# Kernel tuning notes

Hardware: AMD Instinct MI355X
Metric: run time of the kernel (lower is better)

## Reference

```python
import jax, jax.numpy as jnp
import numpy as np

IN_FEATURES = 28 * 28  # 784
OUT_FEATURES = 1000    # label_num
GRID_SIZE = 10
SPLINE_ORDER = 3
GRID_RANGE = (0.0, 1.0)


def _make_grid(dtype):
    # grid = arange(-spline_order, grid_size+spline_order+1) * h + grid_range[0]
    h = (GRID_RANGE[1] - GRID_RANGE[0]) / GRID_SIZE
    return (jnp.arange(-SPLINE_ORDER, GRID_SIZE + SPLINE_ORDER + 1, dtype=dtype) * h
            + GRID_RANGE[0])  # [grid_size + 2*spline_order + 1] = [17]


def b_splines(x):
    # x: [B, in]; returns [B, in, grid_size + spline_order] = [B, 784, 13]
    grid = _make_grid(x.dtype)
    g = grid[None, None, :]          # broadcast over batch and in_features
    xu = x[:, :, None]               # [B, in, 1]
    bases = ((xu >= g[..., :-1]) & (xu < g[..., 1:])).astype(x.dtype)
    for k in range(1, SPLINE_ORDER + 1):
        left = (xu - g[..., :-(k + 1)]) / (g[..., k:-1] - g[..., :-(k + 1)])
        right = (g[..., k + 1:] - xu) / (g[..., k + 1:] - g[..., 1:-k])
        bases = left * bases[..., :-1] + right * bases[..., 1:]
    return bases


def setup_inputs() -> dict:
    key = jax.random.key(0)
    k1, k2, k3, k4 = jax.random.split(key, 4)
    B = 8192
    x = jax.random.uniform(k1, (B, 1, 28, 28), dtype=jnp.float32)  # values in grid range [0,1]
    base_weight = 0.03 * jax.random.normal(k2, (OUT_FEATURES, IN_FEATURES), dtype=jnp.float32)
    spline_weight = 0.02 * jax.random.normal(
        k3, (OUT_FEATURES, IN_FEATURES, GRID_SIZE + SPLINE_ORDER), dtype=jnp.float32)
    spline_scaler = 1.0 + 0.05 * jax.random.normal(k4, (OUT_FEATURES, IN_FEATURES), dtype=jnp.float32)
    return {"x": x, "base_weight": base_weight,
            "spline_weight": spline_weight, "spline_scaler": spline_scaler}


def reference(x, base_weight, spline_weight, spline_scaler):
    B = x.shape[0]
    xf = x.reshape(B, IN_FEATURES)                       # Flatten
    # base branch: SiLU(x) @ base_weight.T
    base_out = jnp.einsum('bi,oi->bo', jax.nn.silu(xf), base_weight)
    # spline branch: B-spline basis contracted with scaled spline weights
    bases = b_splines(xf)                                # [B, in, 13]
    sw = spline_weight * spline_scaler[..., None]        # [out, in, 13]
    spline_out = jnp.einsum('big,oig->bo', bases, sw)
    logits = base_out + spline_out                       # [B, out]
    return jax.nn.log_softmax(logits, axis=1)
```

## Files before the change

kernel.cpp:

```cpp
#include <hip/hip_runtime.h>
#include <hip/hip_bf16.h>
#include <stdint.h>

#define IN_F 784
#define OUT_F 1000
#define CH 16
#define KDIM (IN_F * CH)
#define MDIM 8192
#define NPAD 1024
#define NT (KDIM / 64)
#define BUFSZ 49152

typedef __attribute__((ext_vector_type(8))) short bf16x8;
typedef __attribute__((ext_vector_type(4))) float f32x4;

__device__ __forceinline__ unsigned short f2bf(float f) {
    unsigned u = __float_as_uint(f);
    u = (u + 0x7FFFu + ((u >> 16) & 1u)) >> 16;
    return (unsigned short)u;
}
__device__ __forceinline__ unsigned pack2(float lo, float hi) {
    return (unsigned)f2bf(lo) | ((unsigned)f2bf(hi) << 16);
}

__global__ void prep_A(const float* __restrict__ X, unsigned short* __restrict__ A) {
    int tid = blockIdx.x * 256 + threadIdx.x;
    int b = tid / IN_F;
    int i = tid - b * IN_F;
    float x = X[tid];
    float s = x / (1.0f + __expf(-x));
    float tf = x * 10.0f;
    float cf = floorf(tf);
    cf = fminf(fmaxf(cf, 0.0f), 9.0f);
    int c = (int)cf;
    float u = tf - cf;
    float u2 = u * u, u3 = u2 * u;
    float om = 1.0f - u;
    const float s6 = 1.0f / 6.0f;
    float b0 = om * om * om * s6;
    float b1 = (3.0f * u3 - 6.0f * u2 + 4.0f) * s6;
    float b2 = (-3.0f * u3 + 3.0f * u2 + 3.0f * u + 1.0f) * s6;
    float b3 = u3 * s6;
    float v[16];
    v[0] = s;
    #pragma unroll
    for (int k = 0; k < 13; ++k) {
        float val = (k == c)     ? b0 : 0.0f;
        val       = (k == c + 1) ? b1 : val;
        val       = (k == c + 2) ? b2 : val;
        val       = (k == c + 3) ? b3 : val;
        v[1 + k] = val;
    }
    v[14] = 0.0f; v[15] = 0.0f;
    unsigned w[8];
    #pragma unroll
    for (int j = 0; j < 8; ++j) w[j] = pack2(v[2 * j], v[2 * j + 1]);
    uint4* dst = (uint4*)(A + (size_t)b * KDIM + (size_t)i * CH);
    dst[0] = make_uint4(w[0], w[1], w[2], w[3]);
    dst[1] = make_uint4(w[4], w[5], w[6], w[7]);
}

__global__ void prep_W(const float* __restrict__ BW, const float* __restrict__ SW,
                       const float* __restrict__ SC, unsigned short* __restrict__ Wm) {
    int tid = blockIdx.x * 256 + threadIdx.x;
    int o = tid / IN_F;
    int i = tid - o * IN_F;
    unsigned w[8];
    if (o < OUT_F) {
        float bw = BW[o * IN_F + i];
        float sc = SC[o * IN_F + i];
        const float* swp = SW + (size_t)(o * IN_F + i) * 13;
        float v[16];
        v[0] = bw;
        #pragma unroll
        for (int g = 0; g < 13; ++g) v[1 + g] = swp[g] * sc;
        v[14] = 0.0f; v[15] = 0.0f;
        #pragma unroll
        for (int j = 0; j < 8; ++j) w[j] = pack2(v[2 * j], v[2 * j + 1]);
    } else {
        #pragma unroll
        for (int j = 0; j < 8; ++j) w[j] = 0u;
    }
    uint4* dst = (uint4*)(Wm + (size_t)o * KDIM + (size_t)i * CH);
    dst[0] = make_uint4(w[0], w[1], w[2], w[3]);
    dst[1] = make_uint4(w[4], w[5], w[6], w[7]);
}

__global__ void __launch_bounds__(512, 2) kan_gemm(const unsigned short* __restrict__ A,
                                                   const unsigned short* __restrict__ W,
                                                   float* __restrict__ out) {
    __shared__ __align__(16) unsigned char smem[3 * BUFSZ];
    const int t = threadIdx.x;
    const int bid = blockIdx.x;
    const int sid = ((bid & 7) << 5) + (bid >> 3);
    const int mb = sid >> 3, nb = sid & 7;
    const int bRow = mb << 8, bCol = nb << 7;

    const int lane = t & 63;
    const int w    = t >> 6;
    const int lrow = lane & 15;
    const int lk   = lane >> 4;
    const int sx   = lrow & 7;
    const int wm   = w >> 1, wn = w & 1;
    const int r8   = t >> 3;
    const int p    = t & 7;
    const int lch  = p ^ (r8 & 7);

    const char* srcA[4];
    const char* srcB[2];
    #pragma unroll
    for (int it = 0; it < 4; ++it)
        srcA[it] = (const char*)A + ((size_t)(bRow + it * 64 + r8) * KDIM) * 2 + lch * 16;
    #pragma unroll
    for (int it = 0; it < 2; ++it)
        srcB[it] = (const char*)W + ((size_t)(bCol + it * 64 + r8) * KDIM) * 2 + lch * 16;

    auto stage = [&](int kt, int buf) {
        const size_t ko = (size_t)kt << 7;
        const unsigned db = buf * BUFSZ + t * 16;
        #pragma unroll
        for (int it = 0; it < 4; ++it)
            __builtin_amdgcn_global_load_lds(
                (const __attribute__((address_space(1))) char*)(srcA[it] + ko),
                (__attribute__((address_space(3))) char*)&smem[db + it * 8192],
                16, 0, 0);
        #pragma unroll
        for (int it = 0; it < 2; ++it)
            __builtin_amdgcn_global_load_lds(
                (const __attribute__((address_space(1))) char*)(srcB[it] + ko),
                (__attribute__((address_space(3))) char*)&smem[db + 32768 + it * 8192],
                16, 0, 0);
    };

    f32x4 acc[4][4];
    #pragma unroll
    for (int m = 0; m < 4; ++m)
        #pragma unroll
        for (int n = 0; n < 4; ++n)
            acc[m][n] = (f32x4){0.f, 0.f, 0.f, 0.f};

    stage(0, 0);
    stage(1, 1);

    int cur = 0;
    int nbf = 2;
    for (int kt = 0; kt < NT; ++kt) {
        if (kt < NT - 1) asm volatile("s_waitcnt vmcnt(6)" ::: "memory");
        else             asm volatile("s_waitcnt vmcnt(0)" ::: "memory");
        __builtin_amdgcn_s_barrier();
        asm volatile("" ::: "memory");

        const unsigned char* Abuf = &smem[cur * BUFSZ];
        const unsigned char* Bbuf = Abuf + 32768;
        bf16x8 af[4][2], bfr[4][2];
        #pragma unroll
        for (int m = 0; m < 4; ++m) {
            const int row = (wm << 6) + (m << 4) + lrow;
            #pragma unroll
            for (int kk = 0; kk < 2; ++kk)
                af[m][kk] = *(const bf16x8*)&Abuf[row * 128 + (((kk << 2) + lk) ^ sx) * 16];
        }
        #pragma unroll
        for (int n = 0; n < 4; ++n) {
            const int row = (wn << 6) + (n << 4) + lrow;
            #pragma unroll
            for (int kk = 0; kk < 2; ++kk)
                bfr[n][kk] = *(const bf16x8*)&Bbuf[row * 128 + (((kk << 2) + lk) ^ sx) * 16];
        }

        if (kt + 2 < NT) stage(kt + 2, nbf);

        __builtin_amdgcn_s_setprio(1);
        #pragma unroll
        for (int m = 0; m < 4; ++m)
            #pragma unroll
            for (int n = 0; n < 4; ++n) {
                acc[m][n] = __builtin_amdgcn_mfma_f32_16x16x32_bf16(af[m][0], bfr[n][0], acc[m][n], 0, 0, 0);
                acc[m][n] = __builtin_amdgcn_mfma_f32_16x16x32_bf16(af[m][1], bfr[n][1], acc[m][n], 0, 0, 0);
            }
        __builtin_amdgcn_s_setprio(0);

        cur = (cur == 2) ? 0 : cur + 1;
        nbf = (nbf == 2) ? 0 : nbf + 1;
    }

    #pragma unroll
    for (int m = 0; m < 4; ++m) {
        int grow0 = bRow + (wm << 6) + (m << 4) + (lk << 2);
        #pragma unroll
        for (int n = 0; n < 4; ++n) {
            int gcol = bCol + (wn << 6) + (n << 4) + lrow;
            if (gcol < OUT_F) {
                #pragma unroll
                for (int j = 0; j < 4; ++j)
                    out[(size_t)(grow0 + j) * OUT_F + gcol] = acc[m][n][j];
            }
        }
    }
}

__global__ void logsoftmax_inplace(float* __restrict__ out) {
    const int b = blockIdx.x;
    float* row = out + (size_t)b * OUT_F;
    const int t = threadIdx.x;
    const int ln = t & 63, wv = t >> 6;
    float v[4];
    #pragma unroll
    for (int j = 0; j < 4; ++j) {
        int idx = t + 256 * j;
        v[j] = (idx < OUT_F) ? row[idx] : -1e30f;
    }
    float m = fmaxf(fmaxf(v[0], v[1]), fmaxf(v[2], v[3]));
    #pragma unroll
    for (int off = 32; off > 0; off >>= 1) m = fmaxf(m, __shfl_xor(m, off, 64));
    __shared__ float red[4];
    if (ln == 0) red[wv] = m;
    __syncthreads();
    m = fmaxf(fmaxf(red[0], red[1]), fmaxf(red[2], red[3]));
    float s = 0.f;
    #pragma unroll
    for (int j = 0; j < 4; ++j) {
        int idx = t + 256 * j;
        if (idx < OUT_F) s += __expf(v[j] - m);
    }
    #pragma unroll
    for (int off = 32; off > 0; off >>= 1) s += __shfl_xor(s, off, 64);
    __syncthreads();
    if (ln == 0) red[wv] = s;
    __syncthreads();
    s = red[0] + red[1] + red[2] + red[3];
    float lse = m + logf(s);
    #pragma unroll
    for (int j = 0; j < 4; ++j) {
        int idx = t + 256 * j;
        if (idx < OUT_F) row[idx] = v[j] - lse;
    }
}

extern "C" void kernel_launch(void* const* d_in, const int* in_sizes, int n_in,
                              void* d_out, int out_size, void* d_ws, size_t ws_size,
                              hipStream_t stream) {
    const float* x  = (const float*)d_in[0];
    const float* bw = (const float*)d_in[1];
    const float* sw = (const float*)d_in[2];
    const float* sc = (const float*)d_in[3];
    float* out = (float*)d_out;

    unsigned short* A  = (unsigned short*)d_ws;
    unsigned short* Wm = (unsigned short*)((char*)d_ws + (size_t)MDIM * KDIM * 2);

    prep_A<<<dim3(MDIM * IN_F / 256), 256, 0, stream>>>(x, A);
    prep_W<<<dim3(NPAD * IN_F / 256), 256, 0, stream>>>(bw, sw, sc, Wm);
    kan_gemm<<<dim3((MDIM / 256) * (NPAD / 128)), 512, 0, stream>>>(A, Wm, out);
    logsoftmax_inplace<<<dim3(MDIM), 256, 0, stream>>>(out);
}
```

Before: 373.4 us.

## Software-pipeline LDS fragment reads across K half-steps to overlap with MFMA

Splits each 64-wide K tile into two 32-wide halves and double-buffers the register fragments. The next tile's first half is read from LDS, after its wait and barrier, while the current tile's second-half MFMAs are still outstanding. The goal is to hide LDS read latency and barrier stalls behind matrix math. In exchange it holds more fragment registers, which can lower occupancy, and the wait, barrier and prefetch ordering becomes harder to get right.

```diff
diff --git a/kernel.cpp b/kernel.cpp
--- a/kernel.cpp
+++ b/kernel.cpp
@@ -132,6 +132,21 @@
                 16, 0, 0);
     };
 
+    const int arow = (wm << 6) + lrow;
+    const int brow = (wn << 6) + lrow;
+
+    auto read_half = [&](int buf, int kk, bf16x8 (&af)[4], bf16x8 (&bfr)[4]) {
+        const unsigned char* Abuf = &smem[buf * BUFSZ];
+        const unsigned char* Bbuf = Abuf + 32768;
+        const int ch = (((kk << 2) + lk) ^ sx) * 16;
+        #pragma unroll
+        for (int m = 0; m < 4; ++m)
+            af[m] = *(const bf16x8*)&Abuf[(arow + (m << 4)) * 128 + ch];
+        #pragma unroll
+        for (int n = 0; n < 4; ++n)
+            bfr[n] = *(const bf16x8*)&Bbuf[(brow + (n << 4)) * 128 + ch];
+    };
+
     f32x4 acc[4][4];
     #pragma unroll
     for (int m = 0; m < 4; ++m)
@@ -139,48 +154,48 @@
         for (int n = 0; n < 4; ++n)
             acc[m][n] = (f32x4){0.f, 0.f, 0.f, 0.f};
 
+    bf16x8 afA[4], bfA[4];
+    bf16x8 afB[4], bfB[4];
+
     stage(0, 0);
     stage(1, 1);
+    asm volatile("s_waitcnt vmcnt(6)" ::: "memory");
+    __builtin_amdgcn_s_barrier();
+    asm volatile("" ::: "memory");
+    read_half(0, 0, afA, bfA);
 
     int cur = 0;
     int nbf = 2;
     for (int kt = 0; kt < NT; ++kt) {
-        if (kt < NT - 1) asm volatile("s_waitcnt vmcnt(6)" ::: "memory");
-        else             asm volatile("s_waitcnt vmcnt(0)" ::: "memory");
-        __builtin_amdgcn_s_barrier();
-        asm volatile("" ::: "memory");
-
-        const unsigned char* Abuf = &smem[cur * BUFSZ];
-        const unsigned char* Bbuf = Abuf + 32768;
-        bf16x8 af[4][2], bfr[4][2];
-        #pragma unroll
-        for (int m = 0; m < 4; ++m) {
-            const int row = (wm << 6) + (m << 4) + lrow;
-            #pragma unroll
-            for (int kk = 0; kk < 2; ++kk)
-                af[m][kk] = *(const bf16x8*)&Abuf[row * 128 + (((kk << 2) + lk) ^ sx) * 16];
-        }
-        #pragma unroll
-        for (int n = 0; n < 4; ++n) {
-            const int row = (wn << 6) + (n << 4) + lrow;
-            #pragma unroll
-            for (int kk = 0; kk < 2; ++kk)
-                bfr[n][kk] = *(const bf16x8*)&Bbuf[row * 128 + (((kk << 2) + lk) ^ sx) * 16];
-        }
-
+        read_half(cur, 1, afB, bfB);
         if (kt + 2 < NT) stage(kt + 2, nbf);
 
         __builtin_amdgcn_s_setprio(1);
         #pragma unroll
         for (int m = 0; m < 4; ++m)
             #pragma unroll
-            for (int n = 0; n < 4; ++n) {
-                acc[m][n] = __builtin_amdgcn_mfma_f32_16x16x32_bf16(af[m][0], bfr[n][0], acc[m][n], 0, 0, 0);
-                acc[m][n] = __builtin_amdgcn_mfma_f32_16x16x32_bf16(af[m][1], bfr[n][1], acc[m][n], 0, 0, 0);
-            }
+            for (int n = 0; n < 4; ++n)
+                acc[m][n] = __builtin_amdgcn_mfma_f32_16x16x32_bf16(afA[m], bfA[n], acc[m][n], 0, 0, 0);
         __builtin_amdgcn_s_setprio(0);
 
-        cur = (cur == 2) ? 0 : cur + 1;
+        const int nxt = (cur == 2) ? 0 : cur + 1;
+        if (kt + 1 < NT) {
+            if (kt + 2 < NT) asm volatile("s_waitcnt vmcnt(6)" ::: "memory");
+            else             asm volatile("s_waitcnt vmcnt(0)" ::: "memory");
+            __builtin_amdgcn_s_barrier();
+            asm volatile("" ::: "memory");
+            read_half(nxt, 0, afA, bfA);
+        }
+
+        __builtin_amdgcn_s_setprio(1);
+        #pragma unroll
+        for (int m = 0; m < 4; ++m)
+            #pragma unroll
+            for (int n = 0; n < 4; ++n)
+                acc[m][n] = __builtin_amdgcn_mfma_f32_16x16x32_bf16(afB[m], bfB[n], acc[m][n], 0, 0, 0);
+        __builtin_amdgcn_s_setprio(0);
+
+        cur = nxt;
         nbf = (nbf == 2) ? 0 : nbf + 1;
     }
 
```

Result: slower. 389.3 us (+4.3%).
